# Optimization experiments

Measured on AMD Instinct MI355X. Metric: run time of the kernel, lower is better.

Reference implementation:

```python
import jax, jax.numpy as jnp
import numpy as np

N = 6144   # number of patches (bag size)
L = 1024   # input feature dim
D = 512    # GCN hidden dim
ALPHA = 0.4
THRESH = 0.5


def _layernorm(x, g, b):
    m = jnp.mean(x, axis=-1, keepdims=True)
    v = jnp.mean((x - m) ** 2, axis=-1, keepdims=True)
    return (x - m) / jnp.sqrt(v + 1e-5) * g + b


def _l1rows(x):
    # F.normalize(x, p=1): row-wise L1 normalize with eps=1e-12
    return x / jnp.maximum(jnp.sum(jnp.abs(x), axis=1, keepdims=True), 1e-12)


def _nonlin(x, w1, b1, g, bn, w2, b2):
    h = jax.nn.relu(_layernorm(x @ w1 + b1, g, bn))
    return h @ w2 + b2


def _gcn(x, adj, w, b, g, bn):
    # GraphConvolution: adj @ (x @ W) + bias, then LayerNorm + ReLU
    return jax.nn.relu(_layernorm(adj @ (x @ w) + b, g, bn))


def setup_inputs() -> dict:
    key = jax.random.key(0)
    ks = iter(jax.random.split(key, 64))

    def nrm(shape, s=0.02):
        return jax.random.normal(next(ks), shape, jnp.float32) * s

    inp = {
        'x_path': jax.random.normal(next(ks), (N, L), jnp.float32),
        'maps': jax.random.uniform(next(ks), (N, N), jnp.float32) * 0.1,
    }
    for pre in ['nl0', 'nl1']:
        inp[pre + '_w1'] = nrm((L, D)); inp[pre + '_b1'] = jnp.zeros((D,), jnp.float32)
        inp[pre + '_g'] = jnp.ones((D,), jnp.float32); inp[pre + '_bn'] = jnp.zeros((D,), jnp.float32)
        inp[pre + '_w2'] = nrm((D, D)); inp[pre + '_b2'] = jnp.zeros((D,), jnp.float32)
    for pre in ['gc0', 'gc1', 'gc2', 'ga0', 'ga1', 'ga2']:
        inp[pre + '_w'] = nrm((D, D)); inp[pre + '_b'] = jnp.zeros((D,), jnp.float32)
        inp[pre + '_g'] = jnp.ones((D,), jnp.float32); inp[pre + '_bn'] = jnp.zeros((D,), jnp.float32)
    inp['attn_wa'] = nrm((L, 256)); inp['attn_ba'] = jnp.zeros((256,), jnp.float32)
    inp['attn_wb'] = nrm((L, 256)); inp['attn_bb'] = jnp.zeros((256,), jnp.float32)
    inp['attn_wc'] = nrm((256, 1)); inp['attn_bc'] = jnp.zeros((1,), jnp.float32)
    inp['cls_w'] = nrm((L, 4), 0.001)
    inp['ln_g'] = jnp.ones((L,), jnp.float32); inp['ln_b'] = jnp.zeros((L,), jnp.float32)
    return inp


def reference(x_path, maps,
              nl0_w1, nl0_b1, nl0_g, nl0_bn, nl0_w2, nl0_b2,
              nl1_w1, nl1_b1, nl1_g, nl1_bn, nl1_w2, nl1_b2,
              gc0_w, gc0_b, gc0_g, gc0_bn,
              gc1_w, gc1_b, gc1_g, gc1_bn,
              gc2_w, gc2_b, gc2_g, gc2_bn,
              ga0_w, ga0_b, ga0_g, ga0_bn,
              ga1_w, ga1_b, ga1_g, ga1_bn,
              ga2_w, ga2_b, ga2_g, ga2_bn,
              attn_wa, attn_ba, attn_wb, attn_bb, attn_wc, attn_bc,
              cls_w, ln_g, ln_b):
    # cosine-similarity adjacency: L2-normalize rows, gram matrix, min-max, threshold
    xn = x_path / jnp.maximum(jnp.linalg.norm(x_path, axis=1, keepdims=True), 1e-12)
    cs = xn @ xn.T                                       # [N,N]
    cs = (cs - cs.min()) / (cs.max() - cs.min())
    cs = (cs >= THRESH).astype(jnp.float32)

    # gated attention (eval mode, no dropout): A = Wc (tanh(Wa x) * sigmoid(Wb x))
    a = jnp.tanh(x_path @ attn_wa + attn_ba)
    bg = jax.nn.sigmoid(x_path @ attn_wb + attn_bb)
    agg = (a * bg) @ attn_wc + attn_bc                   # [N,1]

    s = jax.nn.sigmoid(agg)
    aw = s * s.T                                         # outer product [N,N]
    aw = (aw - aw.min()) / (aw.max() - aw.min())
    aw = ALPHA + (1.0 - ALPHA) * aw + maps

    cs = _l1rows(cs)
    aw = _l1rows(aw)

    x0 = _nonlin(x_path, nl0_w1, nl0_b1, nl0_g, nl0_bn, nl0_w2, nl0_b2)
    x1 = _nonlin(x_path, nl1_w1, nl1_b1, nl1_g, nl1_bn, nl1_w2, nl1_b2)

    g1 = _gcn(x0, cs, gc0_w, gc0_b, gc0_g, gc0_bn)
    g1 = _gcn(g1, cs, gc1_w, gc1_b, gc1_g, gc1_bn)
    g1 = _gcn(g1, cs, gc2_w, gc2_b, gc2_g, gc2_bn)

    g2 = _gcn(x1, aw, ga0_w, ga0_b, ga0_g, ga0_bn)
    g2 = _gcn(g2, aw, ga1_w, ga1_b, ga1_g, ga1_bn)
    g2 = _gcn(g2, aw, ga2_w, ga2_b, ga2_g, ga2_bn)

    gcf = jnp.concatenate([g2, g1], axis=1)              # [N, 1024]

    n = x_path.shape[0]
    trans = (cs @ agg) / (n ** 0.5)                      # [N,1]
    fw = jax.nn.softmax(0.3 * trans + 0.7 * agg, axis=0) # softmax over patches
    pooled = fw.T @ gcf                                  # [1, 1024]
    pooled = _layernorm(pooled, ln_g, ln_b)

    logits = pooled @ cls_w                              # [1, 4]
    y_hat = jnp.argmax(logits, axis=1, keepdims=True)    # topk k=1 index
    hazards = jax.nn.sigmoid(logits)
    surv = jnp.cumprod(1.0 - hazards, axis=1)
    return hazards, surv, y_hat
```

## Files before the change

### kernel.cpp

```cpp
#include <hip/hip_runtime.h>

#define N_ 6144
#define L_ 1024
#define D_ 512
#define H_ 256
#define SPARSE_MAX 64u

typedef unsigned short u16;
typedef unsigned long long u64;
typedef __attribute__((ext_vector_type(4))) float f32x4;
typedef __attribute__((ext_vector_type(8))) short s16x8;
typedef __attribute__((ext_vector_type(4))) short s16x4;

__device__ __forceinline__ u16 f2b(float f){
  unsigned u = __float_as_uint(f);
  u += 0x7FFFu + ((u >> 16) & 1u);
  return (u16)(u >> 16);
}
__device__ __forceinline__ float b2f(u16 h){ return __uint_as_float(((unsigned)h) << 16); }
__device__ __forceinline__ unsigned fkey(float f){
  unsigned u = __float_as_uint(f);
  return (u & 0x80000000u) ? ~u : (u | 0x80000000u);
}
__device__ __forceinline__ float funkey(unsigned k){
  unsigned u = (k & 0x80000000u) ? (k & 0x7FFFFFFFu) : ~k;
  return __uint_as_float(u);
}
__device__ __forceinline__ float wave_sum(float v){
  #pragma unroll
  for(int o=32;o;o>>=1) v += __shfl_xor(v,o);
  return v;
}
__device__ __forceinline__ float wave_max(float v){
  #pragma unroll
  for(int o=32;o;o>>=1) v = fmaxf(v,__shfl_xor(v,o));
  return v;
}
__device__ __forceinline__ float wave_min(float v){
  #pragma unroll
  for(int o=32;o;o>>=1) v = fminf(v,__shfl_xor(v,o));
  return v;
}
__device__ __forceinline__ float blk_sum256(float v){
  __shared__ float sm[4];
  v = wave_sum(v);
  __syncthreads();
  if((threadIdx.x&63)==0) sm[threadIdx.x>>6]=v;
  __syncthreads();
  return sm[0]+sm[1]+sm[2]+sm[3];
}
__device__ __forceinline__ float blk_min256(float v){
  __shared__ float sm[4];
  v = wave_min(v);
  __syncthreads();
  if((threadIdx.x&63)==0) sm[threadIdx.x>>6]=v;
  __syncthreads();
  return fminf(fminf(sm[0],sm[1]),fminf(sm[2],sm[3]));
}
__device__ __forceinline__ float blk_max256(float v){
  __shared__ float sm[4];
  v = wave_max(v);
  __syncthreads();
  if((threadIdx.x&63)==0) sm[threadIdx.x>>6]=v;
  __syncthreads();
  return fmaxf(fmaxf(sm[0],sm[1]),fmaxf(sm[2],sm[3]));
}


template<int VW> __device__ __forceinline__ void waitv(){
  if constexpr(VW==8) asm volatile("s_waitcnt vmcnt(8)" ::: "memory");
  else if constexpr(VW==4) asm volatile("s_waitcnt vmcnt(4)" ::: "memory");
  else asm volatile("s_waitcnt vmcnt(0)" ::: "memory");
}

#define STG4(bb,k0) do{ \
  __builtin_amdgcn_global_load_lds((__attribute__((address_space(1))) void*)(gA0+(k0)), (__attribute__((address_space(3))) void*)(lds + (bb)*4096 + (wid<<9)),        16, 0, 0); \
  __builtin_amdgcn_global_load_lds((__attribute__((address_space(1))) void*)(gA1+(k0)), (__attribute__((address_space(3))) void*)(lds + (bb)*4096 + 2048 + (wid<<9)), 16, 0, 0); \
  __builtin_amdgcn_global_load_lds((__attribute__((address_space(1))) void*)(gB0+(k0)), (__attribute__((address_space(3))) void*)(lds + 12288 + (bb)*4096 + (wid<<9)),        16, 0, 0); \
  __builtin_amdgcn_global_load_lds((__attribute__((address_space(1))) void*)(gB1+(k0)), (__attribute__((address_space(3))) void*)(lds + 12288 + (bb)*4096 + 2048 + (wid<<9)), 16, 0, 0); \
}while(0)

template<int MODE>
__global__ __launch_bounds__(256) void gemm_bt(
  const u16* __restrict__ A, const u16* __restrict__ Bt,
  int M, int Nc, int K,
  u16* __restrict__ Cb, unsigned* __restrict__ mmx,
  const unsigned* __restrict__ gate)
{
  if (gate && gate[2] <= SPARSE_MAX) return;
  __shared__ __align__(16) u16 lds[3*4096*2];
  const int tid = threadIdx.x;
  const int wid = tid>>6, lane = tid&63;

  const int gx = gridDim.x;
  int lid = blockIdx.y*gx + blockIdx.x;
  const int nwg = gx*gridDim.y;
  if ((nwg & 7) == 0) {
    const int chunk = nwg >> 3;
    lid = (lid & 7)*chunk + (lid >> 3);
  }
  const int m0 = (lid/gx)<<7, n0 = (lid%gx)<<7;
  const int wr = wid>>1, wc = wid&1;

  const int Klen = K / gridDim.z;
  const int kbeg = blockIdx.z * Klen;

  const int srow = (wid<<4) + (lane>>2);
  const int scol = (((lane&3) ^ ((lane>>2)&3))<<3);
  const u16* gA0 = A  + (size_t)(m0+srow   )*K + scol;
  const u16* gA1 = A  + (size_t)(m0+srow+64)*K + scol;
  const u16* gB0 = Bt + (size_t)(n0+srow   )*K + scol;
  const u16* gB1 = Bt + (size_t)(n0+srow+64)*K + scol;

  f32x4 acc[4][4] = {};
  const int lr = lane&15, lk = (lane>>4)<<3;
  const int rdo = lk ^ ((lr&3)<<3);

  const int NIT = Klen>>5;
  STG4(0, kbeg);
  STG4(1, kbeg+32);
  STG4(2, kbeg+64);

  for (int it=0; it<NIT-2; ++it){
    const int b = it - (it/3)*3;
    waitv<8>();
    __builtin_amdgcn_s_barrier();
    const u16* baseA = lds + b*4096;
    const u16* baseB = lds + 12288 + b*4096;
    s16x8 af[4], bfr[4];
    #pragma unroll
    for(int m=0;m<4;m++) af[m]  = *(const s16x8*)(baseA + ((wr<<6)+(m<<4)+lr)*32 + rdo);
    #pragma unroll
    for(int n=0;n<4;n++) bfr[n] = *(const s16x8*)(baseB + ((wc<<6)+(n<<4)+lr)*32 + rdo);
    asm volatile("s_waitcnt lgkmcnt(0)" ::: "memory");
    __builtin_amdgcn_sched_barrier(0);
    __builtin_amdgcn_s_barrier();
    if (it+3 < NIT) STG4(b, kbeg + ((it+3)<<5));
    #pragma unroll
    for(int m=0;m<4;m++)
      #pragma unroll
      for(int n=0;n<4;n++)
        acc[m][n] = __builtin_amdgcn_mfma_f32_16x16x32_bf16(af[m], bfr[n], acc[m][n], 0,0,0);
  }
  {
    const int it = NIT-2; const int b = it - (it/3)*3;
    waitv<4>();
    __builtin_amdgcn_s_barrier();
    const u16* baseA = lds + b*4096;
    const u16* baseB = lds + 12288 + b*4096;
    s16x8 af[4], bfr[4];
    #pragma unroll
    for(int m=0;m<4;m++) af[m]  = *(const s16x8*)(baseA + ((wr<<6)+(m<<4)+lr)*32 + rdo);
    #pragma unroll
    for(int n=0;n<4;n++) bfr[n] = *(const s16x8*)(baseB + ((wc<<6)+(n<<4)+lr)*32 + rdo);
    #pragma unroll
    for(int m=0;m<4;m++)
      #pragma unroll
      for(int n=0;n<4;n++)
        acc[m][n] = __builtin_amdgcn_mfma_f32_16x16x32_bf16(af[m], bfr[n], acc[m][n], 0,0,0);
  }
  {
    const int it = NIT-1; const int b = it - (it/3)*3;
    waitv<0>();
    __builtin_amdgcn_s_barrier();
    const u16* baseA = lds + b*4096;
    const u16* baseB = lds + 12288 + b*4096;
    s16x8 af[4], bfr[4];
    #pragma unroll
    for(int m=0;m<4;m++) af[m]  = *(const s16x8*)(baseA + ((wr<<6)+(m<<4)+lr)*32 + rdo);
    #pragma unroll
    for(int n=0;n<4;n++) bfr[n] = *(const s16x8*)(baseB + ((wc<<6)+(n<<4)+lr)*32 + rdo);
    #pragma unroll
    for(int m=0;m<4;m++)
      #pragma unroll
      for(int n=0;n<4;n++)
        acc[m][n] = __builtin_amdgcn_mfma_f32_16x16x32_bf16(af[m], bfr[n], acc[m][n], 0,0,0);
  }

  float tmin = 3.0e38f, tmax = -3.0e38f;
  if (MODE==1){
    #pragma unroll
    for(int m=0;m<4;m++)
      #pragma unroll
      for(int n=0;n<4;n++){
        f32x4 v = acc[m][n];
        #pragma unroll
        for(int e=0;e<4;e++){ tmin = fminf(tmin,v[e]); tmax = fmaxf(tmax,v[e]); }
      }
  }

  __syncthreads();
  u16* lC = lds;
  {
    const int rb_l = (wr<<6) + ((lane>>4)<<2);
    const int cb_l = (wc<<6) + lr;
    #pragma unroll
    for(int m=0;m<4;m++)
      #pragma unroll
      for(int n=0;n<4;n++){
        f32x4 v = acc[m][n];
        #pragma unroll
        for(int e=0;e<4;e++)
          lC[(rb_l+(m<<4)+e)*128 + cb_l+(n<<4)] = f2b(v[e]);
      }
  }
  __syncthreads();
  u16* Cp = (MODE==0) ? (Cb + (size_t)blockIdx.z * M * Nc) : Cb;
  #pragma unroll
  for(int q=0;q<8;q++){
    int c = (q<<8) + tid;
    int r = c>>4, cc = (c&15)<<3;
    s16x8 v = *(const s16x8*)(lC + r*128 + cc);
    if (MODE==1)
      __builtin_nontemporal_store(v, (s16x8*)(Cp + (size_t)(m0+r)*Nc + n0 + cc));
    else
      *(s16x8*)(Cp + (size_t)(m0+r)*Nc + n0 + cc) = v;
  }

  if (MODE==1){
    tmin = wave_min(tmin); tmax = wave_max(tmax);
    __shared__ float rmn[4], rmx[4];
    if(lane==0){ rmn[wid]=tmin; rmx[wid]=tmax; }
    __syncthreads();
    if(tid==0){
      float mn=fminf(fminf(rmn[0],rmn[1]),fminf(rmn[2],rmn[3]));
      float mx=fmaxf(fmaxf(rmx[0],rmx[1]),fmaxf(rmx[2],rmx[3]));
      atomicMin(mmx+0, fkey(mn));
      atomicMax(mmx+1, fkey(mx));
    }
  }
}

__global__ __launch_bounds__(256) void transpose_cast(
  const float* __restrict__ src, u16* __restrict__ dst, int R, int C)
{
  __shared__ float t[32][33];
  int c0 = blockIdx.x<<5, r0 = blockIdx.y<<5;
  int tx = threadIdx.x&31, ty = threadIdx.x>>5;
  #pragma unroll
  for(int i=0;i<32;i+=8) t[ty+i][tx] = src[(size_t)(r0+ty+i)*C + c0+tx];
  __syncthreads();
  #pragma unroll
  for(int i=0;i<32;i+=8) dst[(size_t)(c0+ty+i)*R + r0+tx] = f2b(t[tx][ty+i]);
}

__global__ __launch_bounds__(256) void transpose_sum_bf(
  const u16* __restrict__ src, size_t pstr, int nsp,
  u16* __restrict__ dst, int R, int C, const unsigned* __restrict__ gate)
{
  if (gate && gate[2] <= SPARSE_MAX) return;
  __shared__ float t[32][33];
  int c0 = blockIdx.x<<5, r0 = blockIdx.y<<5;
  int tx = threadIdx.x&31, ty = threadIdx.x>>5;
  #pragma unroll
  for(int i=0;i<32;i+=8){
    float v = 0;
    for(int p=0;p<nsp;p++)
      v += b2f(src[(size_t)p*pstr + (size_t)(r0+ty+i)*C + c0+tx]);
    t[ty+i][tx] = v;
  }
  __syncthreads();
  #pragma unroll
  for(int i=0;i<32;i+=8) dst[(size_t)(c0+ty+i)*R + r0+tx] = f2b(t[tx][ty+i]);
}

__global__ __launch_bounds__(256) void prep_x(const float* __restrict__ x,
  u16* __restrict__ xb, u16* __restrict__ xnb)
{
  int row = blockIdx.x, t = threadIdx.x;
  const float* p = x + (size_t)row*L_ + (t<<2);
  f32x4 v = *(const f32x4*)p;
  float ss = v[0]*v[0]+v[1]*v[1]+v[2]*v[2]+v[3]*v[3];
  float tot = blk_sum256(ss);
  float inv = 1.0f/fmaxf(sqrtf(tot), 1e-12f);
  u16* pb = xb  + (size_t)row*L_ + (t<<2);
  u16* pn = xnb + (size_t)row*L_ + (t<<2);
  #pragma unroll
  for(int k=0;k<4;k++){ pb[k]=f2b(v[k]); pn[k]=f2b(v[k]*inv); }
}

__global__ __launch_bounds__(256) void attn_epi(const u16* __restrict__ SPA,
  size_t pstr, int nsp,
  const float* __restrict__ ba, const float* __restrict__ bb,
  const float* __restrict__ wc, const float* __restrict__ bc,
  float* __restrict__ agg, float* __restrict__ s)
{
  int row = (blockIdx.x<<2) + (threadIdx.x>>6);
  int lane = threadIdx.x&63;
  float a[4]={0,0,0,0}, b[4]={0,0,0,0};
  for(int p=0;p<nsp;p++){
    s16x4 ua = *(const s16x4*)(SPA + (size_t)p*pstr + (size_t)row*1536 + (lane<<2));
    s16x4 ub = *(const s16x4*)(SPA + (size_t)p*pstr + (size_t)row*1536 + 256 + (lane<<2));
    #pragma unroll
    for(int j=0;j<4;j++){ a[j]+=b2f((u16)ua[j]); b[j]+=b2f((u16)ub[j]); }
  }
  float acc=0;
  #pragma unroll
  for(int j=0;j<4;j++){
    int h = (lane<<2)+j;
    float tv = tanhf(a[j]+ba[h]);
    float sg = 1.0f/(1.0f+expf(-(b[j]+bb[h])));
    acc += tv*sg*wc[h];
  }
  acc = wave_sum(acc);
  if(lane==0){
    float v = acc + bc[0];
    agg[row]=v;
    s[row]=1.0f/(1.0f+expf(-v));
  }
}

__global__ __launch_bounds__(256) void s_stats(const float* __restrict__ s, float* __restrict__ sc){
  int t=threadIdx.x;
  float sum=0, mn=3e38f, mx=-3e38f;
  for(int i=t;i<N_;i+=256){ float v=s[i]; sum+=v; mn=fminf(mn,v); mx=fmaxf(mx,v); }
  float S=blk_sum256(sum);
  float MN=blk_min256(mn);
  float MX=blk_max256(mx);
  if(t==0){ sc[0]=S; sc[1]=MN; sc[2]=MX; }
}

__global__ __launch_bounds__(256) void aw_write(const float* __restrict__ maps, const float* __restrict__ s,
  const float* __restrict__ sc, u16* __restrict__ awb)
{
  int i = blockIdx.x, t = threadIdx.x;
  float smin = sc[1], smax = sc[2];
  float mn = smin*smin, mx = smax*smax;
  float beta = 0.6f/(mx-mn);
  float c1 = 0.4f - beta*mn;
  float si = s[i];
  const float* mrow = maps + (size_t)i*N_;
  float mv[24];
  float part = 0;
  #pragma unroll
  for(int q=0;q<24;q++){
    int j = t + (q<<8);
    mv[q] = c1 + beta*si*s[j] + mrow[j];
    part += mv[q];
  }
  float r = blk_sum256(part);
  float inv = 1.0f/fmaxf(r, 1e-12f);
  u16* orow = awb + (size_t)i*N_;
  #pragma unroll
  for(int q=0;q<24;q++)
    __builtin_nontemporal_store(f2b(mv[q]*inv), orow + t + (q<<8));
}

__global__ __launch_bounds__(256) void ln_epi512(const u16* __restrict__ Y, size_t pstr, int nsp,
  int rs, int cbase,
  const float* __restrict__ ki,
  const float* __restrict__ bias, const float* __restrict__ g, const float* __restrict__ bn,
  u16* __restrict__ outb,
  const unsigned* __restrict__ gate, const u16* __restrict__ Yalt)
{
  const u16* src = Y; size_t ps = pstr; int np = nsp, rstride = rs, cb = cbase;
  if (gate && gate[2] <= SPARSE_MAX){ src = Yalt; ps = 0; np = 1; rstride = 512; cb = 0; }
  int row = (blockIdx.x<<2)+(threadIdx.x>>6);
  int lane = threadIdx.x&63;
  int c0 = lane<<3;
  float v[8] = {0,0,0,0,0,0,0,0};
  for(int p=0;p<np;p++){
    s16x8 u = *(const s16x8*)(src + (size_t)p*ps + (size_t)row*rstride + cb + c0);
    #pragma unroll
    for(int j=0;j<8;j++) v[j] += b2f((u16)u[j]);
  }
  float scale = ki ? (1.0f/ki[row]) : 1.0f;
  float sum=0, ssum=0;
  #pragma unroll
  for(int j=0;j<8;j++){ v[j] = v[j]*scale + bias[c0+j]; sum+=v[j]; ssum+=v[j]*v[j]; }
  sum = wave_sum(sum); ssum = wave_sum(ssum);
  float m = sum*(1.0f/D_);
  float var = ssum*(1.0f/D_) - m*m;
  float invsd = rsqrtf(var + 1e-5f);
  u16 ob[8];
  #pragma unroll
  for(int j=0;j<8;j++){
    float o = (v[j]-m)*invsd*g[c0+j] + bn[c0+j];
    o = fmaxf(o, 0.0f);
    ob[j] = f2b(o);
  }
  *(s16x8*)(outb + (size_t)row*D_ + c0) = *(s16x8*)ob;
}

__global__ __launch_bounds__(256) void bias_cast(const u16* __restrict__ Y, size_t pstr, int nsp,
  const float* __restrict__ b, u16* __restrict__ outb)
{
  size_t idx = ((size_t)blockIdx.x*256 + threadIdx.x)<<3;
  float v[8] = {0,0,0,0,0,0,0,0};
  for(int p=0;p<nsp;p++){
    s16x8 u = *(const s16x8*)(Y + (size_t)p*pstr + idx);
    #pragma unroll
    for(int j=0;j<8;j++) v[j] += b2f((u16)u[j]);
  }
  int c = (int)(idx & (D_-1));
  u16 ob[8];
  #pragma unroll
  for(int k=0;k<8;k++) ob[k] = f2b(v[k]+b[c+k]);
  *(s16x8*)(outb+idx) = *(s16x8*)ob;
}

__global__ void init_k(unsigned* mmx){ mmx[0]=0xFFFFFFFFu; mmx[1]=0u; mmx[2]=0u; }

__global__ __launch_bounds__(256) void binarize(u16* __restrict__ csb,
  unsigned* __restrict__ mmx, const float* __restrict__ agg,
  float* __restrict__ ki, float* __restrict__ z, u64* __restrict__ bm)
{
  int i = blockIdx.x, t = threadIdx.x;
  int lane = t&63, w = t>>6;
  float mn = funkey(mmx[0]), mx = funkey(mmx[1]);
  float th = mn + 0.5f*(mx-mn);
  u16* row = csb + (size_t)i*N_;
  u64* bmrow = bm + (size_t)i*96;
  float cnt = 0, dot = 0;
  #pragma unroll
  for(int q=0;q<24;q++){
    int j = t + (q<<8);
    bool on = b2f(row[j]) >= th;
    __builtin_nontemporal_store(on ? (u16)0x3F80 : (u16)0, row + j);
    u64 mask = __ballot(on);
    if(lane==0) bmrow[(q<<2)+w] = mask;
    if(on){ cnt += 1.0f; dot += agg[j]; }
  }
  float k = blk_sum256(cnt);
  float dt = blk_sum256(dot);
  if(t==0){
    ki[i] = k;
    float tr = dt/(k*sqrtf((float)N_));
    z[i] = 0.3f*tr + 0.7f*agg[i];
    atomicMax(mmx+2, (unsigned)(k+0.5f));
  }
}

__global__ __launch_bounds__(256) void gather_rows(const u64* __restrict__ bm,
  const u16* __restrict__ SPp, size_t pstr, int nsp,
  const unsigned* __restrict__ gate, u16* __restrict__ YS)
{
  if (gate[2] > SPARSE_MAX) return;
  int i = blockIdx.x, t = threadIdx.x;
  __shared__ u64 wbuf[96];
  __shared__ u16 idx[SPARSE_MAX];
  __shared__ int nn_s;
  if (t < 96) wbuf[t] = bm[(size_t)i*96 + t];
  __syncthreads();
  if (t == 0){
    int nn = 0;
    for(int k=0;k<96;k++){
      u64 m = wbuf[k];
      while(m && nn < (int)SPARSE_MAX){
        int b = __ffsll((long long)m) - 1;
        m &= m - 1;
        idx[nn++] = (u16)((k<<6) + b);
      }
    }
    nn_s = nn;
  }
  __syncthreads();
  int nn = nn_s;
  float a0=0, a1=0;
  for(int k=0;k<nn;k++){
    size_t jb = (size_t)idx[k]*512;
    for(int p=0;p<nsp;p++){
      a0 += b2f(SPp[p*pstr + jb + t]);
      a1 += b2f(SPp[p*pstr + jb + t + 256]);
    }
  }
  YS[(size_t)i*512 + t]       = f2b(a0);
  YS[(size_t)i*512 + t + 256] = f2b(a1);
}

__global__ __launch_bounds__(1024) void softmax_prep(const float* __restrict__ z,
  float* __restrict__ e, float* __restrict__ sexp)
{
  int t = threadIdx.x;
  __shared__ float sm[16];
  float mx=-3e38f;
  for(int i=t;i<N_;i+=1024) mx=fmaxf(mx,z[i]);
  mx = wave_max(mx);
  if((t&63)==0) sm[t>>6]=mx;
  __syncthreads();
  float zm = sm[0];
  #pragma unroll
  for(int w=1;w<16;w++) zm=fmaxf(zm,sm[w]);
  __syncthreads();
  float sum=0;
  for(int i=t;i<N_;i+=1024){ float ee=expf(z[i]-zm); e[i]=ee; sum+=ee; }
  sum = wave_sum(sum);
  if((t&63)==0) sm[t>>6]=sum;
  __syncthreads();
  if(t==0){ float S=0; for(int w=0;w<16;w++) S+=sm[w]; *sexp=S; }
}

__global__ __launch_bounds__(256) void pooled_partial(const float* __restrict__ e,
  const u16* __restrict__ g2b, const u16* __restrict__ g1b, float* __restrict__ part)
{
  int b = blockIdx.x, t = threadIdx.x;
  float a0=0,a1=0,a2=0,a3=0;
  for(int r=0;r<24;r++){
    int row = b*24+r;
    float w = e[row];
    a0 += w * b2f(g2b[(size_t)row*D_ + t]);
    a1 += w * b2f(g2b[(size_t)row*D_ + t+256]);
    a2 += w * b2f(g1b[(size_t)row*D_ + t]);
    a3 += w * b2f(g1b[(size_t)row*D_ + t+256]);
  }
  part[(size_t)b*1024 + t]      = a0;
  part[(size_t)b*1024 + t+256]  = a1;
  part[(size_t)b*1024 + t+512]  = a2;
  part[(size_t)b*1024 + t+768]  = a3;
}

__global__ __launch_bounds__(1024) void final_k(const float* __restrict__ part, const float* __restrict__ sexp,
  const float* __restrict__ lng, const float* __restrict__ lnb,
  const float* __restrict__ clsw, float* __restrict__ out)
{
  int t = threadIdx.x;
  __shared__ float red[16];
  __shared__ float smv[1024];
  __shared__ float lgs[4];
  float p=0;
  for(int b=0;b<256;b++) p += part[b*1024 + t];
  p /= sexp[0];
  float w = wave_sum(p);
  if((t&63)==0) red[t>>6]=w;
  __syncthreads();
  float tot=0;
  #pragma unroll
  for(int i2=0;i2<16;i2++) tot+=red[i2];
  float m = tot*(1.0f/1024.0f);
  __syncthreads();
  float d = p-m;
  w = wave_sum(d*d);
  if((t&63)==0) red[t>>6]=w;
  __syncthreads();
  tot=0;
  #pragma unroll
  for(int i2=0;i2<16;i2++) tot+=red[i2];
  float var = tot*(1.0f/1024.0f);
  float y = d*rsqrtf(var+1e-5f)*lng[t] + lnb[t];
  smv[t]=y;
  __syncthreads();
  if(t<4){
    float lg=0;
    for(int j=0;j<1024;j++) lg += smv[j]*clsw[j*4+t];
    lgs[t]=lg;
  }
  __syncthreads();
  if(t==0){
    float h[4];
    int am=0; float best=lgs[0];
    #pragma unroll
    for(int c2=0;c2<4;c2++){ h[c2]=1.0f/(1.0f+expf(-lgs[c2])); if(lgs[c2]>best){best=lgs[c2];am=c2;} }
    float sv=1.0f;
    #pragma unroll
    for(int c2=0;c2<4;c2++){ out[c2]=h[c2]; sv*=(1.0f-h[c2]); out[4+c2]=sv; }
    out[8]=(float)am;
  }
}

extern "C" void kernel_launch(void* const* d_in, const int* in_sizes, int n_in,
                              void* d_out, int out_size, void* d_ws, size_t ws_size,
                              hipStream_t stream)
{
  const float* x_path =(const float*)d_in[0];
  const float* maps   =(const float*)d_in[1];
  const float* nl0_w1 =(const float*)d_in[2];
  const float* nl0_b1 =(const float*)d_in[3];
  const float* nl0_g  =(const float*)d_in[4];
  const float* nl0_bn =(const float*)d_in[5];
  const float* nl0_w2 =(const float*)d_in[6];
  const float* nl0_b2 =(const float*)d_in[7];
  const float* nl1_w1 =(const float*)d_in[8];
  const float* nl1_b1 =(const float*)d_in[9];
  const float* nl1_g  =(const float*)d_in[10];
  const float* nl1_bn =(const float*)d_in[11];
  const float* nl1_w2 =(const float*)d_in[12];
  const float* nl1_b2 =(const float*)d_in[13];
  const float *gw[6], *gb[6], *gg[6], *gbn[6];
  for(int l=0;l<6;l++){
    gw[l]  = (const float*)d_in[14+l*4+0];
    gb[l]  = (const float*)d_in[14+l*4+1];
    gg[l]  = (const float*)d_in[14+l*4+2];
    gbn[l] = (const float*)d_in[14+l*4+3];
  }
  const float* attn_wa=(const float*)d_in[38];
  const float* attn_ba=(const float*)d_in[39];
  const float* attn_wb=(const float*)d_in[40];
  const float* attn_bb=(const float*)d_in[41];
  const float* attn_wc=(const float*)d_in[42];
  const float* attn_bc=(const float*)d_in[43];
  const float* cls_w  =(const float*)d_in[44];
  const float* ln_g   =(const float*)d_in[45];
  const float* ln_b   =(const float*)d_in[46];

  char* ws=(char*)d_ws;
  size_t off=0;
  auto alc=[&](size_t b)->char*{ char* p=ws+off; off=(off+b+255)&~(size_t)255; return p; };
  u16* BIG = (u16*)alc((size_t)N_*N_*2);
  u16* XB  = (u16*)alc((size_t)N_*L_*2);
  u16* XNB = (u16*)alc((size_t)N_*L_*2);
  u16* WT_proj=(u16*)alc((size_t)1536*L_*2);
  u16* WT_nl0w2=(u16*)alc((size_t)D_*D_*2);
  u16* WT_nl1w2=(u16*)alc((size_t)D_*D_*2);
  u16* WT_g[6];
  for(int l=0;l<6;l++) WT_g[l]=(u16*)alc((size_t)D_*D_*2);
  u16* SP = (u16*)alc((size_t)2*N_*1536*2);
  u16* XWT=(u16*)alc((size_t)D_*N_*2);
  u16* XA0=(u16*)alc((size_t)N_*D_*2);
  u16* XA1=(u16*)alc((size_t)N_*D_*2);
  u16* X0B=(u16*)alc((size_t)N_*D_*2);
  u16* X1B=(u16*)alc((size_t)N_*D_*2);
  u16* YS =(u16*)alc((size_t)N_*D_*2);
  u64* BM =(u64*)alc((size_t)N_*96*8);
  float* PART=(float*)alc((size_t)256*1024*4);
  float* AGG=(float*)alc(N_*4);
  float* SS =(float*)alc(N_*4);
  float* KI =(float*)alc(N_*4);
  float* Z  =(float*)alc(N_*4);
  float* E  =(float*)alc(N_*4);
  float* SC =(float*)alc(256);
  unsigned* MMX=(unsigned*)alc(256);
  float* SEXP=(float*)alc(256);

  const size_t PS_D = (size_t)N_*D_;
  const size_t PS_P = (size_t)N_*1536;

  init_k<<<1,1,0,stream>>>(MMX);
  prep_x<<<N_,256,0,stream>>>(x_path, XB, XNB);

  transpose_cast<<<dim3(H_/32, L_/32),256,0,stream>>>(attn_wa, WT_proj,                         L_, H_);
  transpose_cast<<<dim3(H_/32, L_/32),256,0,stream>>>(attn_wb, WT_proj + (size_t)256*L_,        L_, H_);
  transpose_cast<<<dim3(D_/32, L_/32),256,0,stream>>>(nl0_w1,  WT_proj + (size_t)512*L_,        L_, D_);
  transpose_cast<<<dim3(D_/32, L_/32),256,0,stream>>>(nl1_w1,  WT_proj + (size_t)1024*L_,       L_, D_);
  transpose_cast<<<dim3(D_/32, D_/32),256,0,stream>>>(nl0_w2, WT_nl0w2, D_, D_);
  transpose_cast<<<dim3(D_/32, D_/32),256,0,stream>>>(nl1_w2, WT_nl1w2, D_, D_);
  for(int l=0;l<6;l++)
    transpose_cast<<<dim3(D_/32, D_/32),256,0,stream>>>(gw[l], WT_g[l], D_, D_);

  gemm_bt<0><<<dim3(1536/128, N_/128, 2),256,0,stream>>>(XB, WT_proj, N_, 1536, L_, SP, nullptr, nullptr);
  attn_epi<<<N_/4,256,0,stream>>>(SP, PS_P, 2, attn_ba, attn_bb, attn_wc, attn_bc, AGG, SS);
  s_stats<<<1,256,0,stream>>>(SS,SC);
  aw_write<<<N_,256,0,stream>>>(maps,SS,SC,BIG);

  ln_epi512<<<N_/4,256,0,stream>>>(SP,PS_P,2, 1536,1024, nullptr, nl1_b1,nl1_g,nl1_bn, XA1, nullptr,nullptr);
  ln_epi512<<<N_/4,256,0,stream>>>(SP,PS_P,2, 1536, 512, nullptr, nl0_b1,nl0_g,nl0_bn, XA0, nullptr,nullptr);

  gemm_bt<0><<<dim3(D_/128,N_/128,4),256,0,stream>>>(XA1, WT_nl1w2, N_,D_,D_, SP, nullptr, nullptr);
  bias_cast<<<(N_*D_/8)/256,256,0,stream>>>(SP,PS_D,4, nl1_b2, X1B);

  {
    const u16* cur=X1B;
    for(int l=0;l<3;l++){
      int gi = 3+l;
      gemm_bt<0><<<dim3(D_/128,N_/128,4),256,0,stream>>>(cur, WT_g[gi], N_,D_,D_, SP, nullptr, nullptr);
      transpose_sum_bf<<<dim3(D_/32, N_/32),256,0,stream>>>(SP, PS_D, 4, XWT, N_, D_, nullptr);
      gemm_bt<0><<<dim3(D_/128,N_/128,4),256,0,stream>>>(BIG, XWT, N_,D_,N_, SP, nullptr, nullptr);
      u16* nxt = (l==0)? XA1 : (l==1)? YS : X1B;
      ln_epi512<<<N_/4,256,0,stream>>>(SP,PS_D,4, 512,0, nullptr, gb[gi],gg[gi],gbn[gi], nxt, nullptr,nullptr);
      cur = nxt;
    }
  }

  gemm_bt<0><<<dim3(D_/128,N_/128,4),256,0,stream>>>(XA0, WT_nl0w2, N_,D_,D_, SP, nullptr, nullptr);
  bias_cast<<<(N_*D_/8)/256,256,0,stream>>>(SP,PS_D,4, nl0_b2, X0B);

  gemm_bt<1><<<dim3(N_/128,N_/128,1),256,0,stream>>>(XNB, XNB, N_,N_,L_, BIG, MMX, nullptr);
  binarize<<<N_,256,0,stream>>>(BIG, MMX, AGG, KI, Z, BM);

  {
    const u16* cur=X0B;
    for(int l=0;l<3;l++){
      int gi = l;
      gemm_bt<0><<<dim3(D_/128,N_/128,4),256,0,stream>>>(cur, WT_g[gi], N_,D_,D_, SP, nullptr, nullptr);
      transpose_sum_bf<<<dim3(D_/32, N_/32),256,0,stream>>>(SP, PS_D, 4, XWT, N_, D_, MMX);
      gemm_bt<0><<<dim3(D_/128,N_/128,4),256,0,stream>>>(BIG, XWT, N_,D_,N_, SP, nullptr, MMX);
      gather_rows<<<N_,256,0,stream>>>(BM, SP, PS_D, 4, MMX, YS);
      u16* nxt = (l==0)? XA1 : (l==1)? XA0 : X0B;
      ln_epi512<<<N_/4,256,0,stream>>>(SP,PS_D,4, 512,0, KI, gb[gi],gg[gi],gbn[gi], nxt, MMX, YS);
      cur = nxt;
    }
  }

  softmax_prep<<<1,1024,0,stream>>>(Z,E,SEXP);
  pooled_partial<<<256,256,0,stream>>>(E,X1B,X0B,PART);
  final_k<<<1,1024,0,stream>>>(PART,SEXP,ln_g,ln_b,cls_w,(float*)d_out);

  (void)in_sizes;(void)n_in;(void)out_size;(void)ws_size;
}
```

Before: 869.7 us.

## Exploit Gram symmetry, drop LDS swizzle, split binarize, retune split-K and pooling

The Gram-matrix GEMM (MODE 1) now computes only upper-triangle tiles, and a new mirror_lower kernel transposes them into the lower half, removing nearly half the similarity GEMM's work. The XOR swizzle on LDS staging and reads is removed, which simplifies addressing but may bring back LDS bank conflicts. Binarize no longer writes the 0/1 matrix in place; a separate binarize_store kernel does it only when the dense path is needed. The big adjacency GEMMs move from split-K 4 to 6, and pooled_partial uses 32 blocks instead of 256.

```diff
diff --git a/kernel.cpp b/kernel.cpp
--- a/kernel.cpp
+++ b/kernel.cpp
@@ -65,7 +65,6 @@
   __syncthreads();
   return fmaxf(fmaxf(sm[0],sm[1]),fmaxf(sm[2],sm[3]));
 }
-
 
 template<int VW> __device__ __forceinline__ void waitv(){
   if constexpr(VW==8) asm volatile("s_waitcnt vmcnt(8)" ::: "memory");
@@ -100,13 +99,14 @@
     lid = (lid & 7)*chunk + (lid >> 3);
   }
   const int m0 = (lid/gx)<<7, n0 = (lid%gx)<<7;
+  if (MODE==1 && m0 > n0) return;
   const int wr = wid>>1, wc = wid&1;
 
   const int Klen = K / gridDim.z;
   const int kbeg = blockIdx.z * Klen;
 
   const int srow = (wid<<4) + (lane>>2);
-  const int scol = (((lane&3) ^ ((lane>>2)&3))<<3);
+  const int scol = (lane&3)<<3;
   const u16* gA0 = A  + (size_t)(m0+srow   )*K + scol;
   const u16* gA1 = A  + (size_t)(m0+srow+64)*K + scol;
   const u16* gB0 = Bt + (size_t)(n0+srow   )*K + scol;
@@ -114,7 +114,6 @@
 
   f32x4 acc[4][4] = {};
   const int lr = lane&15, lk = (lane>>4)<<3;
-  const int rdo = lk ^ ((lr&3)<<3);
 
   const int NIT = Klen>>5;
   STG4(0, kbeg);
@@ -129,9 +128,9 @@
     const u16* baseB = lds + 12288 + b*4096;
     s16x8 af[4], bfr[4];
     #pragma unroll
-    for(int m=0;m<4;m++) af[m]  = *(const s16x8*)(baseA + ((wr<<6)+(m<<4)+lr)*32 + rdo);
-    #pragma unroll
-    for(int n=0;n<4;n++) bfr[n] = *(const s16x8*)(baseB + ((wc<<6)+(n<<4)+lr)*32 + rdo);
+    for(int m=0;m<4;m++) af[m]  = *(const s16x8*)(baseA + ((wr<<6)+(m<<4)+lr)*32 + lk);
+    #pragma unroll
+    for(int n=0;n<4;n++) bfr[n] = *(const s16x8*)(baseB + ((wc<<6)+(n<<4)+lr)*32 + lk);
     asm volatile("s_waitcnt lgkmcnt(0)" ::: "memory");
     __builtin_amdgcn_sched_barrier(0);
     __builtin_amdgcn_s_barrier();
@@ -150,9 +149,9 @@
     const u16* baseB = lds + 12288 + b*4096;
     s16x8 af[4], bfr[4];
     #pragma unroll
-    for(int m=0;m<4;m++) af[m]  = *(const s16x8*)(baseA + ((wr<<6)+(m<<4)+lr)*32 + rdo);
-    #pragma unroll
-    for(int n=0;n<4;n++) bfr[n] = *(const s16x8*)(baseB + ((wc<<6)+(n<<4)+lr)*32 + rdo);
+    for(int m=0;m<4;m++) af[m]  = *(const s16x8*)(baseA + ((wr<<6)+(m<<4)+lr)*32 + lk);
+    #pragma unroll
+    for(int n=0;n<4;n++) bfr[n] = *(const s16x8*)(baseB + ((wc<<6)+(n<<4)+lr)*32 + lk);
     #pragma unroll
     for(int m=0;m<4;m++)
       #pragma unroll
@@ -167,9 +166,9 @@
     const u16* baseB = lds + 12288 + b*4096;
     s16x8 af[4], bfr[4];
     #pragma unroll
-    for(int m=0;m<4;m++) af[m]  = *(const s16x8*)(baseA + ((wr<<6)+(m<<4)+lr)*32 + rdo);
-    #pragma unroll
-    for(int n=0;n<4;n++) bfr[n] = *(const s16x8*)(baseB + ((wc<<6)+(n<<4)+lr)*32 + rdo);
+    for(int m=0;m<4;m++) af[m]  = *(const s16x8*)(baseA + ((wr<<6)+(m<<4)+lr)*32 + lk);
+    #pragma unroll
+    for(int n=0;n<4;n++) bfr[n] = *(const s16x8*)(baseB + ((wc<<6)+(n<<4)+lr)*32 + lk);
     #pragma unroll
     for(int m=0;m<4;m++)
       #pragma unroll
@@ -231,6 +230,20 @@
   }
 }
 
+__global__ __launch_bounds__(256) void mirror_lower(u16* __restrict__ C)
+{
+  int c0 = blockIdx.x<<5, r0 = blockIdx.y<<5;
+  if ((r0>>7) >= (c0>>7)) return;
+  __shared__ u16 t[32][33];
+  int tx = threadIdx.x&31, ty = threadIdx.x>>5;
+  #pragma unroll
+  for(int i=0;i<32;i+=8) t[ty+i][tx] = C[(size_t)(r0+ty+i)*N_ + c0+tx];
+  __syncthreads();
+  #pragma unroll
+  for(int i=0;i<32;i+=8)
+    __builtin_nontemporal_store(t[tx][ty+i], C + (size_t)(c0+ty+i)*N_ + r0+tx);
+}
+
 __global__ __launch_bounds__(256) void transpose_cast(
   const float* __restrict__ src, u16* __restrict__ dst, int R, int C)
 {
@@ -401,7 +414,7 @@
 
 __global__ void init_k(unsigned* mmx){ mmx[0]=0xFFFFFFFFu; mmx[1]=0u; mmx[2]=0u; }
 
-__global__ __launch_bounds__(256) void binarize(u16* __restrict__ csb,
+__global__ __launch_bounds__(256) void binarize(const u16* __restrict__ csb,
   unsigned* __restrict__ mmx, const float* __restrict__ agg,
   float* __restrict__ ki, float* __restrict__ z, u64* __restrict__ bm)
 {
@@ -409,14 +422,13 @@
   int lane = t&63, w = t>>6;
   float mn = funkey(mmx[0]), mx = funkey(mmx[1]);
   float th = mn + 0.5f*(mx-mn);
-  u16* row = csb + (size_t)i*N_;
+  const u16* row = csb + (size_t)i*N_;
   u64* bmrow = bm + (size_t)i*96;
   float cnt = 0, dot = 0;
   #pragma unroll
   for(int q=0;q<24;q++){
     int j = t + (q<<8);
     bool on = b2f(row[j]) >= th;
-    __builtin_nontemporal_store(on ? (u16)0x3F80 : (u16)0, row + j);
     u64 mask = __ballot(on);
     if(lane==0) bmrow[(q<<2)+w] = mask;
     if(on){ cnt += 1.0f; dot += agg[j]; }
@@ -428,6 +440,21 @@
     float tr = dt/(k*sqrtf((float)N_));
     z[i] = 0.3f*tr + 0.7f*agg[i];
     atomicMax(mmx+2, (unsigned)(k+0.5f));
+  }
+}
+
+__global__ __launch_bounds__(256) void binarize_store(u16* __restrict__ csb,
+  const unsigned* __restrict__ mmx)
+{
+  if (mmx[2] <= SPARSE_MAX) return;
+  int i = blockIdx.x, t = threadIdx.x;
+  float mn = funkey(mmx[0]), mx = funkey(mmx[1]);
+  float th = mn + 0.5f*(mx-mn);
+  u16* row = csb + (size_t)i*N_;
+  #pragma unroll
+  for(int q=0;q<24;q++){
+    int j = t + (q<<8);
+    row[j] = (b2f(row[j]) >= th) ? (u16)0x3F80 : (u16)0;
   }
 }
 
@@ -495,8 +522,8 @@
 {
   int b = blockIdx.x, t = threadIdx.x;
   float a0=0,a1=0,a2=0,a3=0;
-  for(int r=0;r<24;r++){
-    int row = b*24+r;
+  for(int r=0;r<192;r++){
+    int row = b*192+r;
     float w = e[row];
     a0 += w * b2f(g2b[(size_t)row*D_ + t]);
     a1 += w * b2f(g2b[(size_t)row*D_ + t+256]);
@@ -518,7 +545,7 @@
   __shared__ float smv[1024];
   __shared__ float lgs[4];
   float p=0;
-  for(int b=0;b<256;b++) p += part[b*1024 + t];
+  for(int b=0;b<32;b++) p += part[b*1024 + t];
   p /= sexp[0];
   float w = wave_sum(p);
   if((t&63)==0) red[t>>6]=w;
@@ -611,7 +638,7 @@
   u16* X1B=(u16*)alc((size_t)N_*D_*2);
   u16* YS =(u16*)alc((size_t)N_*D_*2);
   u64* BM =(u64*)alc((size_t)N_*96*8);
-  float* PART=(float*)alc((size_t)256*1024*4);
+  float* PART=(float*)alc((size_t)32*1024*4);
   float* AGG=(float*)alc(N_*4);
   float* SS =(float*)alc(N_*4);
   float* KI =(float*)alc(N_*4);
@@ -627,10 +654,10 @@
   init_k<<<1,1,0,stream>>>(MMX);
   prep_x<<<N_,256,0,stream>>>(x_path, XB, XNB);
 
-  transpose_cast<<<dim3(H_/32, L_/32),256,0,stream>>>(attn_wa, WT_proj,                         L_, H_);
-  transpose_cast<<<dim3(H_/32, L_/32),256,0,stream>>>(attn_wb, WT_proj + (size_t)256*L_,        L_, H_);
-  transpose_cast<<<dim3(D_/32, L_/32),256,0,stream>>>(nl0_w1,  WT_proj + (size_t)512*L_,        L_, D_);
-  transpose_cast<<<dim3(D_/32, L_/32),256,0,stream>>>(nl1_w1,  WT_proj + (size_t)1024*L_,       L_, D_);
+  transpose_cast<<<dim3(H_/32, L_/32),256,0,stream>>>(attn_wa, WT_proj,                   L_, H_);
+  transpose_cast<<<dim3(H_/32, L_/32),256,0,stream>>>(attn_wb, WT_proj + (size_t)256*L_,  L_, H_);
+  transpose_cast<<<dim3(D_/32, L_/32),256,0,stream>>>(nl0_w1,  WT_proj + (size_t)512*L_,  L_, D_);
+  transpose_cast<<<dim3(D_/32, L_/32),256,0,stream>>>(nl1_w1,  WT_proj + (size_t)1024*L_, L_, D_);
   transpose_cast<<<dim3(D_/32, D_/32),256,0,stream>>>(nl0_w2, WT_nl0w2, D_, D_);
   transpose_cast<<<dim3(D_/32, D_/32),256,0,stream>>>(nl1_w2, WT_nl1w2, D_, D_);
   for(int l=0;l<6;l++)
@@ -653,9 +680,9 @@
       int gi = 3+l;
       gemm_bt<0><<<dim3(D_/128,N_/128,4),256,0,stream>>>(cur, WT_g[gi], N_,D_,D_, SP, nullptr, nullptr);
       transpose_sum_bf<<<dim3(D_/32, N_/32),256,0,stream>>>(SP, PS_D, 4, XWT, N_, D_, nullptr);
-      gemm_bt<0><<<dim3(D_/128,N_/128,4),256,0,stream>>>(BIG, XWT, N_,D_,N_, SP, nullptr, nullptr);
+      gemm_bt<0><<<dim3(D_/128,N_/128,6),256,0,stream>>>(BIG, XWT, N_,D_,N_, SP, nullptr, nullptr);
       u16* nxt = (l==0)? XA1 : (l==1)? YS : X1B;
-      ln_epi512<<<N_/4,256,0,stream>>>(SP,PS_D,4, 512,0, nullptr, gb[gi],gg[gi],gbn[gi], nxt, nullptr,nullptr);
+      ln_epi512<<<N_/4,256,0,stream>>>(SP,PS_D,6, 512,0, nullptr, gb[gi],gg[gi],gbn[gi], nxt, nullptr,nullptr);
       cur = nxt;
     }
   }
@@ -663,8 +690,10 @@
   gemm_bt<0><<<dim3(D_/128,N_/128,4),256,0,stream>>>(XA0, WT_nl0w2, N_,D_,D_, SP, nullptr, nullptr);
   bias_cast<<<(N_*D_/8)/256,256,0,stream>>>(SP,PS_D,4, nl0_b2, X0B);
 
-  gemm_bt<1><<<dim3(N_/128,N_/128,1),256,0,stream>>>(XNB, XNB, N_,N_,L_, BIG, MMX, nullptr);
+  gemm_bt<1><<<dim3(N_/128, N_/128, 1),256,0,stream>>>(XNB, XNB, N_,N_,L_, BIG, MMX, nullptr);
+  mirror_lower<<<dim3(N_/32, N_/32),256,0,stream>>>(BIG);
   binarize<<<N_,256,0,stream>>>(BIG, MMX, AGG, KI, Z, BM);
+  binarize_store<<<N_,256,0,stream>>>(BIG, MMX);
 
   {
     const u16* cur=X0B;
@@ -672,16 +701,16 @@
       int gi = l;
       gemm_bt<0><<<dim3(D_/128,N_/128,4),256,0,stream>>>(cur, WT_g[gi], N_,D_,D_, SP, nullptr, nullptr);
       transpose_sum_bf<<<dim3(D_/32, N_/32),256,0,stream>>>(SP, PS_D, 4, XWT, N_, D_, MMX);
-      gemm_bt<0><<<dim3(D_/128,N_/128,4),256,0,stream>>>(BIG, XWT, N_,D_,N_, SP, nullptr, MMX);
+      gemm_bt<0><<<dim3(D_/128,N_/128,6),256,0,stream>>>(BIG, XWT, N_,D_,N_, SP, nullptr, MMX);
       gather_rows<<<N_,256,0,stream>>>(BM, SP, PS_D, 4, MMX, YS);
       u16* nxt = (l==0)? XA1 : (l==1)? XA0 : X0B;
-      ln_epi512<<<N_/4,256,0,stream>>>(SP,PS_D,4, 512,0, KI, gb[gi],gg[gi],gbn[gi], nxt, MMX, YS);
+      ln_epi512<<<N_/4,256,0,stream>>>(SP,PS_D,6, 512,0, KI, gb[gi],gg[gi],gbn[gi], nxt, MMX, YS);
       cur = nxt;
     }
   }
 
   softmax_prep<<<1,1024,0,stream>>>(Z,E,SEXP);
-  pooled_partial<<<256,256,0,stream>>>(E,X1B,X0B,PART);
+  pooled_partial<<<32,256,0,stream>>>(E,X1B,X0B,PART);
   final_k<<<1,1024,0,stream>>>(PART,SEXP,ln_g,ln_b,cls_w,(float*)d_out);
 
   (void)in_sizes;(void)n_in;(void)out_size;(void)ws_size;
```

New measurement: 877.5 us. Within noise of the previous version (+0.9%).
